# Performance work log

Hardware: AMD Instinct MI355X
Metric: run time of the kernel (lower is better)

Reference implementation:

```python
import jax, jax.numpy as jnp
import numpy as np

N_NODES = 100000
HID = 64
IN_DIM = 128


def setup_inputs() -> dict:
    key = jax.random.key(0)
    ks = jax.random.split(key, 12)
    x = jax.random.normal(ks[0], (N_NODES, IN_DIM), dtype=jnp.float32)
    edge_index = jax.random.randint(ks[1], (2, 1600000), 0, N_NODES, dtype=jnp.int64)
    batch = jnp.zeros((N_NODES,), dtype=jnp.int64)
    def glorot(k, shape):
        fan_in, fan_out = shape
        lim = (6.0 / (fan_in + fan_out)) ** 0.5
        return jax.random.uniform(k, shape, jnp.float32, -lim, lim)
    return {
        "x": x,
        "edge_index": edge_index,
        "batch": batch,
        "W1": glorot(ks[2], (IN_DIM, HID)), "b1": jnp.zeros((HID,), jnp.float32),
        "W2": glorot(ks[3], (HID, HID)),   "b2": jnp.zeros((HID,), jnp.float32),
        "W3": glorot(ks[4], (HID, HID)),   "b3": jnp.zeros((HID,), jnp.float32),
        "Wp1": glorot(ks[5], (HID, HID // 2)), "bp1": jnp.zeros((HID // 2,), jnp.float32),
        "Wp2": glorot(ks[6], (HID // 2, 1)),   "bp2": jnp.zeros((1,), jnp.float32),
    }


def _gcn_norm(edge_index, n_nodes):
    # Add self-loops, compute symmetric normalization deg^{-1/2}[src]*deg^{-1/2}[dst]
    loops = jnp.arange(n_nodes, dtype=edge_index.dtype)
    src = jnp.concatenate([edge_index[0], loops])
    dst = jnp.concatenate([edge_index[1], loops])
    deg = jax.ops.segment_sum(jnp.ones_like(dst, dtype=jnp.float32), dst,
                              num_segments=n_nodes)
    dinv = jnp.where(deg > 0, jax.lax.rsqrt(deg), 0.0)
    norm = dinv[src] * dinv[dst]  # [E + N]
    return src, dst, norm


def _gcn_layer(x, src, dst, norm, W, b, n_nodes):
    h = x @ W                       # [N, out]  dense transform first (PyG order)
    msg = h[src] * norm[:, None]    # gather + scale, [E+N, out]
    agg = jax.ops.segment_sum(msg, dst, num_segments=n_nodes)  # scatter-add
    return agg + b


def reference(x, edge_index, batch, W1, b1, W2, b2, W3, b3, Wp1, bp1, Wp2, bp2):
    n = x.shape[0]
    src, dst, norm = _gcn_norm(edge_index, n)
    # eval mode: dropout is identity
    h = jax.nn.relu(_gcn_layer(x, src, dst, norm, W1, b1, n))
    h = jax.nn.relu(_gcn_layer(h, src, dst, norm, W2, b2, n))
    h = jax.nn.relu(_gcn_layer(h, src, dst, norm, W3, b3, n))
    h = jax.nn.relu(h @ Wp1 + bp1)
    return h @ Wp2 + bp2  # [N, 1] node predictions
```

## Files before the change

kernel.cpp:

```cpp
#include <hip/hip_runtime.h>
#include <hip/hip_bf16.h>
#include <hip/hip_fp16.h>

#define NDIM_IN 128
#define HID 64

#define BINW 128
#define NB   782
#define NC   256
#define CAP  3072

typedef _Float16 f16x8 __attribute__((ext_vector_type(8)));
typedef float f32x4 __attribute__((ext_vector_type(4)));

__global__ __launch_bounds__(1024) void hist_k(const int* __restrict__ dst,
                                               int* __restrict__ histT, int E) {
  __shared__ int h[NB];
  for (int i = threadIdx.x; i < NB; i += 1024) h[i] = 0;
  __syncthreads();
  int E4 = E >> 2;
  int chunk = (E4 + NC - 1) / NC;
  int beg = blockIdx.x * chunk;
  int end = min(E4, beg + chunk);
  const int4* __restrict__ d4 = (const int4*)dst;
  for (int i = beg + (int)threadIdx.x; i < end; i += 1024) {
    int4 d = d4[i];
    atomicAdd(&h[d.x >> 7], 1);
    atomicAdd(&h[d.y >> 7], 1);
    atomicAdd(&h[d.z >> 7], 1);
    atomicAdd(&h[d.w >> 7], 1);
  }
  __syncthreads();
  for (int i = threadIdx.x; i < NB; i += 1024)
    histT[i * NC + blockIdx.x] = h[i];
}

__global__ __launch_bounds__(256) void scan1(int* __restrict__ g,
                                             int* __restrict__ bs, int len) {
  __shared__ int s[256];
  int t = threadIdx.x;
  int i = blockIdx.x * 256 + t;
  int v = (i < len) ? g[i] : 0;
  s[t] = v;
  __syncthreads();
  for (int off = 1; off < 256; off <<= 1) {
    int x = (t >= off) ? s[t - off] : 0;
    __syncthreads();
    s[t] += x;
    __syncthreads();
  }
  if (i < len) g[i] = s[t] - v;
  if (t == 255) bs[blockIdx.x] = s[255];
}

__global__ __launch_bounds__(1024) void scan2(int* __restrict__ bs, int nb) {
  __shared__ int s[1024];
  int t = threadIdx.x;
  int v = (t < nb) ? bs[t] : 0;
  s[t] = v;
  __syncthreads();
  for (int off = 1; off < 1024; off <<= 1) {
    int x = (t >= off) ? s[t - off] : 0;
    __syncthreads();
    s[t] += x;
    __syncthreads();
  }
  if (t < nb) bs[t] = s[t] - v;
}

__global__ __launch_bounds__(1024) void scatter_k(const int* __restrict__ src,
                                                  const int* __restrict__ dst,
                                                  const int* __restrict__ S,
                                                  const int* __restrict__ bsum,
                                                  int* __restrict__ tmp, int E) {
  __shared__ int cur[NB];
  for (int i = threadIdx.x; i < NB; i += 1024)
    cur[i] = S[i * NC + blockIdx.x] + bsum[i];
  __syncthreads();
  int E4 = E >> 2;
  int chunk = (E4 + NC - 1) / NC;
  int beg = blockIdx.x * chunk;
  int end = min(E4, beg + chunk);
  const int4* __restrict__ d4 = (const int4*)dst;
  const int4* __restrict__ s4 = (const int4*)src;
  for (int i = beg + (int)threadIdx.x; i < end; i += 1024) {
    int4 d = d4[i];
    int4 sv = s4[i];
    int p0 = atomicAdd(&cur[d.x >> 7], 1); tmp[p0] = (sv.x << 7) | (d.x & 127);
    int p1 = atomicAdd(&cur[d.y >> 7], 1); tmp[p1] = (sv.y << 7) | (d.y & 127);
    int p2 = atomicAdd(&cur[d.z >> 7], 1); tmp[p2] = (sv.z << 7) | (d.z & 127);
    int p3 = atomicAdd(&cur[d.w >> 7], 1); tmp[p3] = (sv.w << 7) | (d.w & 127);
  }
}

__global__ __launch_bounds__(256) void binsort_k(const int* __restrict__ tmp,
                                                 const int* __restrict__ bsum,
                                                 int* __restrict__ col,
                                                 int* __restrict__ rp,
                                                 float* __restrict__ dinv,
                                                 int n, int E) {
  int bin = blockIdx.x;
  int base = bsum[bin];
  int end = (bin == NB - 1) ? E : bsum[bin + 1];
  int m = end - base;
  __shared__ int cnt[BINW];
  __shared__ int offs[BINW];
  __shared__ int cur[BINW];
  __shared__ int buf[CAP];
  int t = threadIdx.x;
  if (t < BINW) cnt[t] = 0;
  __syncthreads();
  for (int i = t; i < m; i += 256) {
    int p = tmp[base + i];
    atomicAdd(&cnt[p & (BINW - 1)], 1);
  }
  __syncthreads();
  if (t < BINW) offs[t] = cnt[t];
  __syncthreads();
  for (int off = 1; off < BINW; off <<= 1) {
    int x = (t < BINW && t >= off) ? offs[t - off] : 0;
    __syncthreads();
    if (t < BINW) offs[t] += x;
    __syncthreads();
  }
  if (t < BINW) {
    int ex = offs[t] - cnt[t];
    cur[t] = ex;
    int v = bin * BINW + t;
    if (v < n) {
      rp[v] = base + ex;
      dinv[v] = rsqrtf((float)cnt[t] + 1.0f);
    }
  }
  if (bin == NB - 1 && t == 0) rp[n] = E;
  __syncthreads();
  for (int i = t; i < m; i += 256) {
    int p = tmp[base + i];
    int r = atomicAdd(&cur[p & (BINW - 1)], 1);
    if (r < CAP) buf[r] = p >> 7;
  }
  __syncthreads();
  int mm = min(m, CAP);
  for (int i = t; i < mm; i += 256) col[base + i] = buf[i];
}

template <int K, int FP16IN>
__global__ __launch_bounds__(256) void gemm_mfma(const void* __restrict__ Xv,
                                                 const float* __restrict__ W,
                                                 const float* __restrict__ dinv,
                                                 __half* __restrict__ T,
                                                 int n, int ntiles) {
  constexpr int NCH = K / 32;
  __shared__ float Ds[4][16 * 68];
  int wv = threadIdx.x >> 6;
  int lane = threadIdx.x & 63;
  int colx = lane & 15;
  int quad = lane >> 4;

  f16x8 bf[4][NCH];
#pragma unroll
  for (int t = 0; t < 4; t++)
#pragma unroll
    for (int c = 0; c < NCH; c++) {
      f16x8 b;
#pragma unroll
      for (int j = 0; j < 8; j++)
        b[j] = (_Float16)W[(32 * c + quad * 8 + j) * 64 + 16 * t + colx];
      bf[t][c] = b;
    }

  for (int tile = blockIdx.x * 4 + wv; tile < ntiles; tile += gridDim.x * 4) {
    int node0 = tile * 16;
    f32x4 acc[4] = {{0.f, 0.f, 0.f, 0.f}, {0.f, 0.f, 0.f, 0.f},
                    {0.f, 0.f, 0.f, 0.f}, {0.f, 0.f, 0.f, 0.f}};
    int arow = min(node0 + colx, n - 1);
#pragma unroll
    for (int c = 0; c < NCH; c++) {
      f16x8 a;
      if constexpr (FP16IN) {
        const _Float16* __restrict__ xr = (const _Float16*)Xv + (size_t)arow * K;
        a = *(const f16x8*)(xr + 32 * c + quad * 8);
      } else {
        const float* __restrict__ xr = (const float*)Xv + (size_t)arow * K;
        float4 x0 = *(const float4*)(xr + 32 * c + quad * 8);
        float4 x1 = *(const float4*)(xr + 32 * c + quad * 8 + 4);
        a[0] = (_Float16)x0.x; a[1] = (_Float16)x0.y;
        a[2] = (_Float16)x0.z; a[3] = (_Float16)x0.w;
        a[4] = (_Float16)x1.x; a[5] = (_Float16)x1.y;
        a[6] = (_Float16)x1.z; a[7] = (_Float16)x1.w;
      }
#pragma unroll
      for (int t = 0; t < 4; t++)
        acc[t] = __builtin_amdgcn_mfma_f32_16x16x32_f16(a, bf[t][c], acc[t], 0, 0, 0);
    }
    float dv[4];
#pragma unroll
    for (int r = 0; r < 4; r++) {
      int nd = min(node0 + quad * 4 + r, n - 1);
      dv[r] = dinv[nd];
    }
#pragma unroll
    for (int t = 0; t < 4; t++)
#pragma unroll
      for (int r = 0; r < 4; r++)
        Ds[wv][(quad * 4 + r) * 68 + 16 * t + colx] = acc[t][r] * dv[r];
    int nd = node0 + colx;
    const float* __restrict__ row = &Ds[wv][colx * 68 + quad * 16];
    float4 y0 = *(const float4*)(row + 0);
    float4 y1 = *(const float4*)(row + 4);
    float4 y2 = *(const float4*)(row + 8);
    float4 y3 = *(const float4*)(row + 12);
    f16x8 o0, o1;
    o0[0] = (_Float16)y0.x; o0[1] = (_Float16)y0.y;
    o0[2] = (_Float16)y0.z; o0[3] = (_Float16)y0.w;
    o0[4] = (_Float16)y1.x; o0[5] = (_Float16)y1.y;
    o0[6] = (_Float16)y1.z; o0[7] = (_Float16)y1.w;
    o1[0] = (_Float16)y2.x; o1[1] = (_Float16)y2.y;
    o1[2] = (_Float16)y2.z; o1[3] = (_Float16)y2.w;
    o1[4] = (_Float16)y3.x; o1[5] = (_Float16)y3.y;
    o1[6] = (_Float16)y3.z; o1[7] = (_Float16)y3.w;
    if (nd < n) {
      uint4* __restrict__ o = (uint4*)(T + (size_t)nd * 64 + quad * 16);
      o[0] = *(uint4*)&o0;
      o[1] = *(uint4*)&o1;
    }
  }
}

template <int MODE>
__global__ __launch_bounds__(256) void spmm_relu(const int* __restrict__ rp,
                                                 const int* __restrict__ col,
                                                 const __half* __restrict__ T,
                                                 const float* __restrict__ dinv,
                                                 const float* __restrict__ bias,
                                                 void* __restrict__ Hout, int n) {
  int lane = threadIdx.x & 63;
  int wv = threadIdx.x >> 6;
  int g = lane >> 3;
  int sub = lane & 7;
  int v = blockIdx.x * 32 + wv * 8 + g;
  bool valid = v < n;
  if (!valid) v = n - 1;
  const uint4* __restrict__ T8 = (const uint4*)T;
  int beg = rp[v];
  int end = rp[v + 1];

  float a0[8], a1[8];
  {
    uint4 w = T8[(size_t)v * 8 + sub];
    const __half2* h = (const __half2*)&w;
#pragma unroll
    for (int j = 0; j < 4; j++) {
      float2 f = __half22float2(h[j]);
      a0[2 * j] = f.x; a0[2 * j + 1] = f.y;
      a1[2 * j] = 0.f; a1[2 * j + 1] = 0.f;
    }
  }
  int e = beg;
  for (; e + 2 <= end; e += 2) {
    int s0 = col[e];
    int s1 = col[e + 1];
    uint4 w0 = T8[(size_t)s0 * 8 + sub];
    uint4 w1 = T8[(size_t)s1 * 8 + sub];
    const __half2* h0 = (const __half2*)&w0;
    const __half2* h1 = (const __half2*)&w1;
#pragma unroll
    for (int j = 0; j < 4; j++) {
      float2 f0 = __half22float2(h0[j]);
      float2 f1 = __half22float2(h1[j]);
      a0[2 * j] += f0.x; a0[2 * j + 1] += f0.y;
      a1[2 * j] += f1.x; a1[2 * j + 1] += f1.y;
    }
  }
  if (e < end) {
    int s0 = col[e];
    uint4 w0 = T8[(size_t)s0 * 8 + sub];
    const __half2* h0 = (const __half2*)&w0;
#pragma unroll
    for (int j = 0; j < 4; j++) {
      float2 f0 = __half22float2(h0[j]);
      a0[2 * j] += f0.x; a0[2 * j + 1] += f0.y;
    }
  }
  float di = dinv[v];
  const float4* __restrict__ b4 = (const float4*)bias;
  float4 bA = b4[sub * 2], bB = b4[sub * 2 + 1];
  float4 rA, rB;
  rA.x = di * (a0[0] + a1[0]) + bA.x;
  rA.y = di * (a0[1] + a1[1]) + bA.y;
  rA.z = di * (a0[2] + a1[2]) + bA.z;
  rA.w = di * (a0[3] + a1[3]) + bA.w;
  rB.x = di * (a0[4] + a1[4]) + bB.x;
  rB.y = di * (a0[5] + a1[5]) + bB.y;
  rB.z = di * (a0[6] + a1[6]) + bB.z;
  rB.w = di * (a0[7] + a1[7]) + bB.w;
  rA.x = rA.x > 0.f ? rA.x : 0.f;  rA.y = rA.y > 0.f ? rA.y : 0.f;
  rA.z = rA.z > 0.f ? rA.z : 0.f;  rA.w = rA.w > 0.f ? rA.w : 0.f;
  rB.x = rB.x > 0.f ? rB.x : 0.f;  rB.y = rB.y > 0.f ? rB.y : 0.f;
  rB.z = rB.z > 0.f ? rB.z : 0.f;  rB.w = rB.w > 0.f ? rB.w : 0.f;
  if (valid) {
    if constexpr (MODE == 0) {
      f16x8 o;
      o[0] = (_Float16)rA.x; o[1] = (_Float16)rA.y;
      o[2] = (_Float16)rA.z; o[3] = (_Float16)rA.w;
      o[4] = (_Float16)rB.x; o[5] = (_Float16)rB.y;
      o[6] = (_Float16)rB.z; o[7] = (_Float16)rB.w;
      uint4* __restrict__ o4 = (uint4*)((__half*)Hout + (size_t)v * HID + sub * 8);
      *o4 = *(uint4*)&o;
    } else {
      float4* __restrict__ o = (float4*)((float*)Hout + (size_t)v * HID + sub * 8);
      o[0] = rA;
      o[1] = rB;
    }
  }
}

__global__ __launch_bounds__(256) void mlp_head(const float* __restrict__ H,
                                                const float* __restrict__ Wp1,
                                                const float* __restrict__ bp1,
                                                const float* __restrict__ Wp2,
                                                const float* __restrict__ bp2,
                                                float* __restrict__ out, int n) {
  __shared__ float W1t[32 * 64];
  __shared__ float w2s[32];
  __shared__ float b1s[32];
  for (int i = threadIdx.x; i < 64 * 32; i += 256) {
    int k = i >> 5, j = i & 31;
    W1t[j * 64 + k] = Wp1[i];
  }
  if (threadIdx.x < 32) {
    w2s[threadIdx.x] = Wp2[threadIdx.x];
    b1s[threadIdx.x] = bp1[threadIdx.x];
  }
  __syncthreads();
  int node = blockIdx.x * 256 + threadIdx.x;
  if (node >= n) return;
  float4 h[16];
  const float4* __restrict__ hr = (const float4*)(H + (size_t)node * 64);
#pragma unroll
  for (int j = 0; j < 16; j++) h[j] = hr[j];
  float o = bp2[0];
#pragma unroll
  for (int j = 0; j < 32; j++) {
    const float4* wr = (const float4*)(W1t + j * 64);
    float4 a4 = make_float4(0.f, 0.f, 0.f, 0.f);
#pragma unroll
    for (int k = 0; k < 16; k++) {
      float4 w = wr[k];
      a4.x += h[k].x * w.x;
      a4.y += h[k].y * w.y;
      a4.z += h[k].z * w.z;
      a4.w += h[k].w * w.w;
    }
    float a = a4.x + a4.y + a4.z + a4.w + b1s[j];
    a = a > 0.f ? a : 0.f;
    o += a * w2s[j];
  }
  out[node] = o;
}

extern "C" void kernel_launch(void* const* d_in, const int* in_sizes, int n_in,
                              void* d_out, int out_size, void* d_ws, size_t ws_size,
                              hipStream_t stream) {
  const float* x   = (const float*)d_in[0];
  const int* edge  = (const int*)d_in[1];
  const float* W1  = (const float*)d_in[3];
  const float* b1  = (const float*)d_in[4];
  const float* W2  = (const float*)d_in[5];
  const float* b2  = (const float*)d_in[6];
  const float* W3  = (const float*)d_in[7];
  const float* b3  = (const float*)d_in[8];
  const float* Wp1 = (const float*)d_in[9];
  const float* bp1 = (const float*)d_in[10];
  const float* Wp2 = (const float*)d_in[11];
  const float* bp2 = (const float*)d_in[12];
  float* out = (float*)d_out;

  const int n = in_sizes[0] / NDIM_IN;
  const int E = in_sizes[1] / 2;
  const int* src = edge;
  const int* dst = edge + E;

  char* ws = (char*)d_ws;
  size_t off = 0;
  auto carve = [&](size_t bytes) {
    char* p = ws + off;
    off = (off + bytes + 255) & ~(size_t)255;
    return p;
  };
  int*    histT = (int*)carve((size_t)NB * NC * 4);
  int*    bsum  = (int*)carve(1024 * 4);
  int*    tmp   = (int*)carve((size_t)E * 4);
  int*    col   = (int*)carve((size_t)E * 4);
  int*    rp    = (int*)carve(((size_t)n + 1) * 4);
  float*  dinv  = (float*)carve((size_t)n * 4);
  __half* bufT  = (__half*)carve((size_t)n * HID * 2);
  float*  bufA  = (float*)carve((size_t)n * HID * 4);
  __half* bufH  = (__half*)bufA;
  (void)ws_size; (void)n_in; (void)out_size;

  const int nbN = (n + 255) / 256;
  const int ntiles = (n + 15) >> 4;
  const int nbM = 782;
  const int scan_len = NB * NC;
  const int nbScan = (scan_len + 255) / 256;

  hist_k<<<NC, 1024, 0, stream>>>(dst, histT, E);
  scan1<<<nbScan, 256, 0, stream>>>(histT, bsum, scan_len);
  scan2<<<1, 1024, 0, stream>>>(bsum, nbScan);
  scatter_k<<<NC, 1024, 0, stream>>>(src, dst, histT, bsum, tmp, E);
  binsort_k<<<NB, 256, 0, stream>>>(tmp, bsum, col, rp, dinv, n, E);

  const int nbSp = (n + 31) / 32;

  gemm_mfma<128, 0><<<nbM, 256, 0, stream>>>(x, W1, dinv, bufT, n, ntiles);
  spmm_relu<0><<<nbSp, 256, 0, stream>>>(rp, col, bufT, dinv, b1, bufH, n);
  gemm_mfma<64, 1><<<nbM, 256, 0, stream>>>(bufH, W2, dinv, bufT, n, ntiles);
  spmm_relu<0><<<nbSp, 256, 0, stream>>>(rp, col, bufT, dinv, b2, bufH, n);
  gemm_mfma<64, 1><<<nbM, 256, 0, stream>>>(bufH, W3, dinv, bufT, n, ntiles);
  spmm_relu<1><<<nbSp, 256, 0, stream>>>(rp, col, bufT, dinv, b3, bufA, n);
  mlp_head<<<nbN, 256, 0, stream>>>(bufA, Wp1, bp1, Wp2, bp2, out, n);
}
```

Baseline: 199.8 us.

## Fuse MLP head into final SpMM and unroll neighbor gather by four

The final aggregation kernel now stages each block's 32 node rows in shared memory and computes the two-layer prediction head in place. This removes the separate head kernel and the full fp32 hidden-state round trip through global memory. The neighbor gather loop is unrolled to four independent loads and accumulators to raise memory-level parallelism. The cost is that the fused head runs on only 32 threads per block while the other waves wait. There is also extra shared memory and register pressure.

After: 247.4 us. 23.8% more time.

```diff
diff --git a/kernel.cpp b/kernel.cpp
--- a/kernel.cpp
+++ b/kernel.cpp
@@ -233,7 +233,26 @@
                                                  const __half* __restrict__ T,
                                                  const float* __restrict__ dinv,
                                                  const float* __restrict__ bias,
-                                                 void* __restrict__ Hout, int n) {
+                                                 void* __restrict__ Hout,
+                                                 const float* __restrict__ Wp1,
+                                                 const float* __restrict__ bp1,
+                                                 const float* __restrict__ Wp2,
+                                                 const float* __restrict__ bp2,
+                                                 int n) {
+  __shared__ float Hs[MODE == 2 ? 32 : 1][MODE == 2 ? 68 : 1];
+  __shared__ float W1t[MODE == 2 ? 2048 : 1];
+  __shared__ float w2s[32];
+  __shared__ float b1s[32];
+  if constexpr (MODE == 2) {
+    for (int i = threadIdx.x; i < 64 * 32; i += 256) {
+      int k = i >> 5, j = i & 31;
+      W1t[j * 64 + k] = Wp1[i];
+    }
+    if (threadIdx.x < 32) {
+      w2s[threadIdx.x] = Wp2[threadIdx.x];
+      b1s[threadIdx.x] = bp1[threadIdx.x];
+    }
+  }
   int lane = threadIdx.x & 63;
   int wv = threadIdx.x >> 6;
   int g = lane >> 3;
@@ -245,7 +264,7 @@
   int beg = rp[v];
   int end = rp[v + 1];
 
-  float a0[8], a1[8];
+  float a0[8], a1[8], a2[8], a3[8];
   {
     uint4 w = T8[(size_t)v * 8 + sub];
     const __half2* h = (const __half2*)&w;
@@ -254,25 +273,37 @@
       float2 f = __half22float2(h[j]);
       a0[2 * j] = f.x; a0[2 * j + 1] = f.y;
       a1[2 * j] = 0.f; a1[2 * j + 1] = 0.f;
+      a2[2 * j] = 0.f; a2[2 * j + 1] = 0.f;
+      a3[2 * j] = 0.f; a3[2 * j + 1] = 0.f;
     }
   }
   int e = beg;
-  for (; e + 2 <= end; e += 2) {
+  for (; e + 4 <= end; e += 4) {
     int s0 = col[e];
     int s1 = col[e + 1];
+    int s2 = col[e + 2];
+    int s3 = col[e + 3];
     uint4 w0 = T8[(size_t)s0 * 8 + sub];
     uint4 w1 = T8[(size_t)s1 * 8 + sub];
+    uint4 w2 = T8[(size_t)s2 * 8 + sub];
+    uint4 w3 = T8[(size_t)s3 * 8 + sub];
     const __half2* h0 = (const __half2*)&w0;
     const __half2* h1 = (const __half2*)&w1;
+    const __half2* h2 = (const __half2*)&w2;
+    const __half2* h3 = (const __half2*)&w3;
 #pragma unroll
     for (int j = 0; j < 4; j++) {
       float2 f0 = __half22float2(h0[j]);
       float2 f1 = __half22float2(h1[j]);
+      float2 f2 = __half22float2(h2[j]);
+      float2 f3 = __half22float2(h3[j]);
       a0[2 * j] += f0.x; a0[2 * j + 1] += f0.y;
       a1[2 * j] += f1.x; a1[2 * j + 1] += f1.y;
-    }
-  }
-  if (e < end) {
+      a2[2 * j] += f2.x; a2[2 * j + 1] += f2.y;
+      a3[2 * j] += f3.x; a3[2 * j + 1] += f3.y;
+    }
+  }
+  for (; e < end; ++e) {
     int s0 = col[e];
     uint4 w0 = T8[(size_t)s0 * 8 + sub];
     const __half2* h0 = (const __half2*)&w0;
@@ -286,20 +317,21 @@
   const float4* __restrict__ b4 = (const float4*)bias;
   float4 bA = b4[sub * 2], bB = b4[sub * 2 + 1];
   float4 rA, rB;
-  rA.x = di * (a0[0] + a1[0]) + bA.x;
-  rA.y = di * (a0[1] + a1[1]) + bA.y;
-  rA.z = di * (a0[2] + a1[2]) + bA.z;
-  rA.w = di * (a0[3] + a1[3]) + bA.w;
-  rB.x = di * (a0[4] + a1[4]) + bB.x;
-  rB.y = di * (a0[5] + a1[5]) + bB.y;
-  rB.z = di * (a0[6] + a1[6]) + bB.z;
-  rB.w = di * (a0[7] + a1[7]) + bB.w;
+  rA.x = di * ((a0[0] + a1[0]) + (a2[0] + a3[0])) + bA.x;
+  rA.y = di * ((a0[1] + a1[1]) + (a2[1] + a3[1])) + bA.y;
+  rA.z = di * ((a0[2] + a1[2]) + (a2[2] + a3[2])) + bA.z;
+  rA.w = di * ((a0[3] + a1[3]) + (a2[3] + a3[3])) + bA.w;
+  rB.x = di * ((a0[4] + a1[4]) + (a2[4] + a3[4])) + bB.x;
+  rB.y = di * ((a0[5] + a1[5]) + (a2[5] + a3[5])) + bB.y;
+  rB.z = di * ((a0[6] + a1[6]) + (a2[6] + a3[6])) + bB.z;
+  rB.w = di * ((a0[7] + a1[7]) + (a2[7] + a3[7])) + bB.w;
   rA.x = rA.x > 0.f ? rA.x : 0.f;  rA.y = rA.y > 0.f ? rA.y : 0.f;
   rA.z = rA.z > 0.f ? rA.z : 0.f;  rA.w = rA.w > 0.f ? rA.w : 0.f;
   rB.x = rB.x > 0.f ? rB.x : 0.f;  rB.y = rB.y > 0.f ? rB.y : 0.f;
   rB.z = rB.z > 0.f ? rB.z : 0.f;  rB.w = rB.w > 0.f ? rB.w : 0.f;
-  if (valid) {
-    if constexpr (MODE == 0) {
+
+  if constexpr (MODE == 0) {
+    if (valid) {
       f16x8 o;
       o[0] = (_Float16)rA.x; o[1] = (_Float16)rA.y;
       o[2] = (_Float16)rA.z; o[3] = (_Float16)rA.w;
@@ -307,56 +339,41 @@
       o[6] = (_Float16)rB.z; o[7] = (_Float16)rB.w;
       uint4* __restrict__ o4 = (uint4*)((__half*)Hout + (size_t)v * HID + sub * 8);
       *o4 = *(uint4*)&o;
-    } else {
-      float4* __restrict__ o = (float4*)((float*)Hout + (size_t)v * HID + sub * 8);
-      o[0] = rA;
-      o[1] = rB;
-    }
-  }
-}
-
-__global__ __launch_bounds__(256) void mlp_head(const float* __restrict__ H,
-                                                const float* __restrict__ Wp1,
-                                                const float* __restrict__ bp1,
-                                                const float* __restrict__ Wp2,
-                                                const float* __restrict__ bp2,
-                                                float* __restrict__ out, int n) {
-  __shared__ float W1t[32 * 64];
-  __shared__ float w2s[32];
-  __shared__ float b1s[32];
-  for (int i = threadIdx.x; i < 64 * 32; i += 256) {
-    int k = i >> 5, j = i & 31;
-    W1t[j * 64 + k] = Wp1[i];
-  }
-  if (threadIdx.x < 32) {
-    w2s[threadIdx.x] = Wp2[threadIdx.x];
-    b1s[threadIdx.x] = bp1[threadIdx.x];
-  }
-  __syncthreads();
-  int node = blockIdx.x * 256 + threadIdx.x;
-  if (node >= n) return;
-  float4 h[16];
-  const float4* __restrict__ hr = (const float4*)(H + (size_t)node * 64);
-#pragma unroll
-  for (int j = 0; j < 16; j++) h[j] = hr[j];
-  float o = bp2[0];
-#pragma unroll
-  for (int j = 0; j < 32; j++) {
-    const float4* wr = (const float4*)(W1t + j * 64);
-    float4 a4 = make_float4(0.f, 0.f, 0.f, 0.f);
-#pragma unroll
-    for (int k = 0; k < 16; k++) {
-      float4 w = wr[k];
-      a4.x += h[k].x * w.x;
-      a4.y += h[k].y * w.y;
-      a4.z += h[k].z * w.z;
-      a4.w += h[k].w * w.w;
-    }
-    float a = a4.x + a4.y + a4.z + a4.w + b1s[j];
-    a = a > 0.f ? a : 0.f;
-    o += a * w2s[j];
-  }
-  out[node] = o;
+    }
+  } else {
+    int ln = wv * 8 + g;
+    *(float4*)&Hs[ln][sub * 8] = rA;
+    *(float4*)&Hs[ln][sub * 8 + 4] = rB;
+    __syncthreads();
+    int t = threadIdx.x;
+    if (t < 32) {
+      int node = blockIdx.x * 32 + t;
+      if (node < n) {
+        float4 h[16];
+        const float4* __restrict__ hr = (const float4*)&Hs[t][0];
+#pragma unroll
+        for (int j = 0; j < 16; j++) h[j] = hr[j];
+        float o = bp2[0];
+#pragma unroll
+        for (int j = 0; j < 32; j++) {
+          const float4* wr = (const float4*)(W1t + j * 64);
+          float4 a4 = make_float4(0.f, 0.f, 0.f, 0.f);
+#pragma unroll
+          for (int k = 0; k < 16; k++) {
+            float4 w = wr[k];
+            a4.x += h[k].x * w.x;
+            a4.y += h[k].y * w.y;
+            a4.z += h[k].z * w.z;
+            a4.w += h[k].w * w.w;
+          }
+          float a = a4.x + a4.y + a4.z + a4.w + b1s[j];
+          a = a > 0.f ? a : 0.f;
+          o += a * w2s[j];
+        }
+        ((float*)Hout)[node] = o;
+      }
+    }
+  }
 }
 
 extern "C" void kernel_launch(void* const* d_in, const int* in_sizes, int n_in,
@@ -395,11 +412,9 @@
   int*    rp    = (int*)carve(((size_t)n + 1) * 4);
   float*  dinv  = (float*)carve((size_t)n * 4);
   __half* bufT  = (__half*)carve((size_t)n * HID * 2);
-  float*  bufA  = (float*)carve((size_t)n * HID * 4);
-  __half* bufH  = (__half*)bufA;
+  __half* bufH  = (__half*)carve((size_t)n * HID * 2);
   (void)ws_size; (void)n_in; (void)out_size;
 
-  const int nbN = (n + 255) / 256;
   const int ntiles = (n + 15) >> 4;
   const int nbM = 782;
   const int scan_len = NB * NC;
@@ -414,10 +429,12 @@
   const int nbSp = (n + 31) / 32;
 
   gemm_mfma<128, 0><<<nbM, 256, 0, stream>>>(x, W1, dinv, bufT, n, ntiles);
-  spmm_relu<0><<<nbSp, 256, 0, stream>>>(rp, col, bufT, dinv, b1, bufH, n);
+  spmm_relu<0><<<nbSp, 256, 0, stream>>>(rp, col, bufT, dinv, b1, bufH,
+                                         nullptr, nullptr, nullptr, nullptr, n);
   gemm_mfma<64, 1><<<nbM, 256, 0, stream>>>(bufH, W2, dinv, bufT, n, ntiles);
-  spmm_relu<0><<<nbSp, 256, 0, stream>>>(rp, col, bufT, dinv, b2, bufH, n);
+  spmm_relu<0><<<nbSp, 256, 0, stream>>>(rp, col, bufT, dinv, b2, bufH,
+                                         nullptr, nullptr, nullptr, nullptr, n);
   gemm_mfma<64, 1><<<nbM, 256, 0, stream>>>(bufH, W3, dinv, bufT, n, ntiles);
-  spmm_relu<1><<<nbSp, 256, 0, stream>>>(rp, col, bufT, dinv, b3, bufA, n);
-  mlp_head<<<nbN, 256, 0, stream>>>(bufA, Wp1, bp1, Wp2, bp2, out, n);
-}
+  spmm_relu<2><<<nbSp, 256, 0, stream>>>(rp, col, bufT, dinv, b3, out,
+                                         Wp1, bp1, Wp2, bp2, n);
+}
```
